# Performance work log

Measured on AMD Instinct MI355X. Metric: run time of the kernel, lower is better.

The kernel has to match this reference:

```python
import jax, jax.numpy as jnp
import numpy as np

H_DIM = 32
EPS = 1e-7


def setup_inputs() -> dict:
    key = jax.random.key(0)
    ks = jax.random.split(key, 9)
    B, L, I = 2048, 256, 8
    return {
        "X": jax.random.normal(ks[0], (B, L, I), dtype=jnp.float32),
        "y": jax.random.randint(ks[1], (B,), 0, 2, dtype=jnp.int64),
        "W1": jax.random.normal(ks[2], (I, H_DIM), dtype=jnp.float32),
        "cls_tok": jax.random.normal(ks[3], (H_DIM,), dtype=jnp.float32),
        "W_q": jax.random.normal(ks[4], (H_DIM, H_DIM), dtype=jnp.float32),
        "W_k": jax.random.normal(ks[5], (H_DIM, H_DIM), dtype=jnp.float32),
        "W_v": jax.random.normal(ks[6], (H_DIM, H_DIM), dtype=jnp.float32),
        "W_t": jax.random.normal(ks[7], (H_DIM, H_DIM), dtype=jnp.float32),
        "W2": jax.random.normal(ks[8], (H_DIM, 2), dtype=jnp.float32),
    }


def reference(X, y, W1, cls_tok, W_q, W_k, W_v, W_t, W2):
    B = X.shape[0]
    # global mean/std normalization (torch.std is unbiased, ddof=1)
    h_pre1 = (X - X.mean()) / (X.std(ddof=1) + EPS)
    h_1 = h_pre1 @ W1                                   # [B, L, H]
    cls = jnp.broadcast_to(cls_tok[None, None, :], (B, 1, H_DIM))
    h_pre2 = jnp.concatenate([h_1, cls], axis=1)        # [B, L+1, H]
    Q = h_pre2 @ W_q
    K = h_pre2 @ W_k
    V = h_pre2 @ W_v
    S = jax.nn.softmax(jnp.einsum('bqh,bkh->bqk', Q, K) / jnp.sqrt(jnp.float32(H_DIM)), axis=-1)
    h_2 = jnp.einsum('bqk,bkh->bqh', S, V) + h_pre2 @ W_t
    z = h_2[:, -1] @ W2                                 # [B, o_dim]
    log_s = jax.nn.log_softmax(z, axis=-1)
    loss = -jnp.take_along_axis(log_s, y[:, None], axis=1)[:, 0].mean()
    return loss
```

## Files before the change

### kernel.cpp

```cpp
#include <hip/hip_runtime.h>

#define N_TOTAL 4194304
#define B_SIZE  2048
#define L_SIZE  256
#define I_DIM   8
#define H       32
#define K1_BLK  256
#define K2_BLK  256

#define CRAW_OFF 1024
#define ACC_OFF  1040
#define FIXSCALE 4294967296.0
#define MASK56   0x00FFFFFFFFFFFFFFull

__global__ __launch_bounds__(1024) void k1_stats(
    const float4* __restrict__ X4,
    const float* __restrict__ W1, const float* __restrict__ cls,
    const float* __restrict__ Wq, const float* __restrict__ Wk,
    const float* __restrict__ Wv, const float* __restrict__ Wt,
    const float* __restrict__ W2, double* __restrict__ dws)
{
    const int t = threadIdx.x, b = blockIdx.x;
    const int lane = t & 63, wid = t >> 6;
    const int g = b * 1024 + t;

    float s1 = 0.f, s2 = 0.f;
    #pragma unroll
    for (int i = 0; i < 4; i++) {
        float4 v = X4[g + i * 262144];
        s1 += v.x + v.y + v.z + v.w;
        s2 += v.x * v.x + v.y * v.y + v.z * v.z + v.w * v.w;
    }
    for (int off = 32; off; off >>= 1) {
        s1 += __shfl_down(s1, off);
        s2 += __shfl_down(s2, off);
    }
    __shared__ float a1[16], a2[16];
    if (lane == 0) { a1[wid] = s1; a2[wid] = s2; }
    __syncthreads();
    if (t == 0) {
        float r1 = 0.f, r2 = 0.f;
        #pragma unroll
        for (int i = 0; i < 16; i++) { r1 += a1[i]; r2 += a2[i]; }
        dws[2 * b]     = (double)r1;
        dws[2 * b + 1] = (double)r2;
    }

    if (b == 0) {
        __shared__ float qv[H], kcls[H], vcls[H], tv[H], gg[H], WV[I_DIM][H];
        const float rs32 = 0.17677669529663687f;
        float* craw = (float*)(dws + CRAW_OFF);
        if (t < H) {
            const int h = t;
            float q_ = 0.f, k_ = 0.f, v_ = 0.f, t_ = 0.f;
            for (int j = 0; j < H; j++) {
                float cj = cls[j];
                q_ += cj * Wq[j * H + h];
                k_ += cj * Wk[j * H + h];
                v_ += cj * Wv[j * H + h];
                t_ += cj * Wt[j * H + h];
            }
            qv[h] = q_; kcls[h] = k_; vcls[h] = v_; tv[h] = t_;
        }
        __syncthreads();
        if (t < H) {
            const int h = t;
            float g_ = 0.f;
            for (int j = 0; j < H; j++) g_ += Wk[h * H + j] * qv[j];
            gg[h] = g_;
            for (int i = 0; i < I_DIM; i++) {
                float a = 0.f;
                for (int j = 0; j < H; j++) a += W1[i * H + j] * Wv[j * H + h];
                WV[i][h] = a;
            }
        }
        __syncthreads();
        if (t < I_DIM) {
            float a = 0.f;
            for (int j = 0; j < H; j++) a += W1[t * H + j] * gg[j];
            craw[t] = a;
        }
        if (t < I_DIM * 2) {
            const int i = t >> 1, o = t & 1;
            float a = 0.f;
            for (int j = 0; j < H; j++) a += WV[i][j] * W2[j * 2 + o];
            craw[10 + i * 2 + o] = a;
        }
        if (t == 0) {
            float c2 = 0.f;
            for (int j = 0; j < H; j++) c2 += qv[j] * kcls[j];
            craw[9] = c2 * rs32;
            float vw0 = 0.f, vw1 = 0.f, tw0 = 0.f, tw1 = 0.f;
            for (int j = 0; j < H; j++) {
                vw0 += vcls[j] * W2[j * 2];     vw1 += vcls[j] * W2[j * 2 + 1];
                tw0 += tv[j]   * W2[j * 2];     tw1 += tv[j]   * W2[j * 2 + 1];
            }
            craw[28] = vw0; craw[29] = vw1; craw[30] = tw0; craw[31] = tw1;
            *(unsigned long long*)(dws + ACC_OFF) = 0ull;
        }
    }
}

__global__ __launch_bounds__(1024) void k2_attn(
    const float* __restrict__ X, const int* __restrict__ y,
    double* __restrict__ dws, float* __restrict__ out)
{
    const int t = threadIdx.x, b = blockIdx.x;
    const int lane = t & 63, w = t >> 6;
    const int lr = w >> 1, half = w & 1;
    const int r = b * 8 + lr;

    const float4* Xb = (const float4*)X + (size_t)r * 512;
    const int p0 = half * 128 + lane;
    float4 A = Xb[2 * p0],        Bv = Xb[2 * p0 + 1];
    float4 C = Xb[2 * (p0 + 64)], D  = Xb[2 * (p0 + 64) + 1];

    __shared__ double da[4], db[4];
    if (t < 256) {
        double d1 = dws[2 * t], d2 = dws[2 * t + 1];
        for (int off = 32; off; off >>= 1) {
            d1 += __shfl_down(d1, off);
            d2 += __shfl_down(d2, off);
        }
        if (lane == 0) { da[w] = d1; db[w] = d2; }
    }
    __syncthreads();

    __shared__ float sNegMu, sSdev;
    if (t == 0) {
        double S1 = da[0] + da[1] + da[2] + da[3];
        double S2 = db[0] + db[1] + db[2] + db[3];
        double mu = S1 / (double)N_TOTAL;
        double var = (S2 - S1 * S1 / (double)N_TOTAL) / (double)(N_TOTAL - 1);
        sSdev = (float)(sqrt(var) + 1e-7);
        sNegMu = (float)(-mu);
    }
    __syncthreads();

    __shared__ float cst[32];
    const float* craw = (const float*)(dws + CRAW_OFF);
    const float rs32 = 0.17677669529663687f;
    if (t < 32) {
        const float sdev = sSdev, negmu = sNegMu;
        if (t < 8) {
            cst[t] = craw[t] / sdev * rs32;
        } else if (t == 8) {
            float cs = 0.f;
            for (int i = 0; i < 8; i++) cs += craw[i] / sdev * rs32;
            cst[8] = negmu * cs;
        } else if (t == 9) {
            cst[9] = craw[9];
        } else if (t < 26) {
            cst[t] = craw[t] / sdev;
        } else if (t == 26) {
            float m0 = 0.f;
            for (int i = 0; i < 8; i++) m0 += craw[10 + 2 * i] / sdev;
            cst[26] = negmu * m0;
        } else if (t == 27) {
            float m1 = 0.f;
            for (int i = 0; i < 8; i++) m1 += craw[11 + 2 * i] / sdev;
            cst[27] = negmu * m1;
        } else {
            cst[t] = craw[t];
        }
    }
    __syncthreads();

    float x0[8] = {A.x, A.y, A.z, A.w, Bv.x, Bv.y, Bv.z, Bv.w};
    float x1[8] = {C.x, C.y, C.z, C.w, D.x,  D.y,  D.z,  D.w};
    const float c8 = cst[8];
    float sc0 = c8, sc1 = c8;
    #pragma unroll
    for (int i = 0; i < 8; i++) {
        sc0 += x0[i] * cst[i];
        sc1 += x1[i] * cst[i];
    }

    __shared__ float rmax[8][2];
    __shared__ float rsum[8][2][9];
    __shared__ double wloss[8];
    float mw = fmaxf(sc0, sc1);
    for (int off = 32; off; off >>= 1) mw = fmaxf(mw, __shfl_xor(mw, off));
    if (lane == 0) rmax[lr][half] = mw;
    __syncthreads();
    const float m = fmaxf(fmaxf(rmax[lr][0], rmax[lr][1]), cst[9]);

    float e0 = expf(sc0 - m), e1 = expf(sc1 - m);
    float v[9];
    v[0] = e0 + e1;
    #pragma unroll
    for (int i = 0; i < 8; i++) v[i + 1] = e0 * x0[i] + e1 * x1[i];
    for (int off = 32; off; off >>= 1) {
        #pragma unroll
        for (int j = 0; j < 9; j++) v[j] += __shfl_down(v[j], off);
    }
    if (lane == 0) {
        #pragma unroll
        for (int j = 0; j < 9; j++) rsum[lr][half][j] = v[j];
    }
    __syncthreads();

    if (t < 8) {
        float vv[9];
        #pragma unroll
        for (int j = 0; j < 9; j++) vv[j] = rsum[t][0][j] + rsum[t][1][j];
        float mrow = fmaxf(fmaxf(rmax[t][0], rmax[t][1]), cst[9]);
        float ecls = expf(cst[9] - mrow);
        float inv = 1.f / (vv[0] + ecls);
        float S256 = ecls * inv;
        float z[2];
        #pragma unroll
        for (int o = 0; o < 2; o++) {
            float a = 0.f;
            #pragma unroll
            for (int i = 0; i < 8; i++)
                a += (vv[i + 1] * inv) * cst[10 + i * 2 + o];
            z[o] = a + (1.f - S256) * cst[26 + o] + S256 * cst[28 + o] + cst[30 + o];
        }
        float zm = fmaxf(z[0], z[1]);
        float lse = zm + logf(expf(z[0] - zm) + expf(z[1] - zm));
        int yb = y[b * 8 + t];
        wloss[t] = (double)(lse - z[yb]);
    }
    __syncthreads();

    if (t == 0) {
        double blockloss = 0.0;
        #pragma unroll
        for (int i = 0; i < 8; i++) blockloss += wloss[i];
        unsigned long long fixed =
            (unsigned long long)(blockloss * FIXSCALE + 0.5);
        unsigned long long* acc = (unsigned long long*)(dws + ACC_OFF);
        unsigned long long old = __hip_atomic_fetch_add(
            acc, fixed + (1ull << 56), __ATOMIC_RELAXED, __HIP_MEMORY_SCOPE_AGENT);
        if ((old >> 56) == (unsigned long long)(K2_BLK - 1)) {
            unsigned long long total = ((old & MASK56) + fixed) & MASK56;
            out[0] = (float)((double)total / FIXSCALE / (double)B_SIZE);
        }
    }
}

extern "C" void kernel_launch(void* const* d_in, const int* in_sizes, int n_in,
                              void* d_out, int out_size, void* d_ws, size_t ws_size,
                              hipStream_t stream) {
    const float* X   = (const float*)d_in[0];
    const int*   y   = (const int*)d_in[1];
    const float* W1  = (const float*)d_in[2];
    const float* cls = (const float*)d_in[3];
    const float* Wq  = (const float*)d_in[4];
    const float* Wk  = (const float*)d_in[5];
    const float* Wv  = (const float*)d_in[6];
    const float* Wt  = (const float*)d_in[7];
    const float* W2  = (const float*)d_in[8];
    float* out = (float*)d_out;
    double* dws = (double*)d_ws;

    hipLaunchKernelGGL(k1_stats, dim3(K1_BLK), dim3(1024), 0, stream,
                       (const float4*)X, W1, cls, Wq, Wk, Wv, Wt, W2, dws);
    hipLaunchKernelGGL(k2_attn, dim3(K2_BLK), dim3(1024), 0, stream,
                       X, y, dws, out);
}
```

Measured before the change: 23.02 us.

## Fuse stats and attention into one cooperative kernel with grid barrier

Merges the statistics pass and the attention/loss pass into a single cooperatively launched kernel. Each block loads its X rows into registers once, uses them for the global sum/sumsq, then waits on an atomic arrival counter before reusing the same registers for attention. This removes the second kernel launch and the second read of X. Every block now also recomputes the weight folding redundantly, and a memset is added to clear the counter. A two-kernel fallback with a 512-thread attention kernel is kept in case the cooperative launch fails.

```diff
diff --git a/kernel.cpp b/kernel.cpp
--- a/kernel.cpp
+++ b/kernel.cpp
@@ -5,143 +5,79 @@
 #define L_SIZE  256
 #define I_DIM   8
 #define H       32
-#define K1_BLK  256
-#define K2_BLK  256
-
-#define CRAW_OFF 1024
-#define ACC_OFF  1040
-#define FIXSCALE 4294967296.0
-#define MASK56   0x00FFFFFFFFFFFFFFull
-
-__global__ __launch_bounds__(1024) void k1_stats(
-    const float4* __restrict__ X4,
+#define NBLK    256
+
+#define ARR_BYTE  4160
+#define ACC_BYTE  4168
+#define CRAW_OFF  524
+#define FIXSCALE  4294967296.0
+#define MASK56    0x00FFFFFFFFFFFFFFull
+
+__device__ __forceinline__ void fold_raw(
+    int t,
     const float* __restrict__ W1, const float* __restrict__ cls,
     const float* __restrict__ Wq, const float* __restrict__ Wk,
     const float* __restrict__ Wv, const float* __restrict__ Wt,
-    const float* __restrict__ W2, double* __restrict__ dws)
+    const float* __restrict__ W2,
+    float* qv, float* kcls, float* vcls, float* tv, float* gg,
+    float (*WV)[H], float* craw)
 {
-    const int t = threadIdx.x, b = blockIdx.x;
-    const int lane = t & 63, wid = t >> 6;
-    const int g = b * 1024 + t;
-
-    float s1 = 0.f, s2 = 0.f;
-    #pragma unroll
-    for (int i = 0; i < 4; i++) {
-        float4 v = X4[g + i * 262144];
-        s1 += v.x + v.y + v.z + v.w;
-        s2 += v.x * v.x + v.y * v.y + v.z * v.z + v.w * v.w;
-    }
-    for (int off = 32; off; off >>= 1) {
-        s1 += __shfl_down(s1, off);
-        s2 += __shfl_down(s2, off);
-    }
-    __shared__ float a1[16], a2[16];
-    if (lane == 0) { a1[wid] = s1; a2[wid] = s2; }
-    __syncthreads();
-    if (t == 0) {
-        float r1 = 0.f, r2 = 0.f;
-        #pragma unroll
-        for (int i = 0; i < 16; i++) { r1 += a1[i]; r2 += a2[i]; }
-        dws[2 * b]     = (double)r1;
-        dws[2 * b + 1] = (double)r2;
-    }
-
-    if (b == 0) {
-        __shared__ float qv[H], kcls[H], vcls[H], tv[H], gg[H], WV[I_DIM][H];
-        const float rs32 = 0.17677669529663687f;
-        float* craw = (float*)(dws + CRAW_OFF);
-        if (t < H) {
-            const int h = t;
-            float q_ = 0.f, k_ = 0.f, v_ = 0.f, t_ = 0.f;
-            for (int j = 0; j < H; j++) {
-                float cj = cls[j];
-                q_ += cj * Wq[j * H + h];
-                k_ += cj * Wk[j * H + h];
-                v_ += cj * Wv[j * H + h];
-                t_ += cj * Wt[j * H + h];
-            }
-            qv[h] = q_; kcls[h] = k_; vcls[h] = v_; tv[h] = t_;
-        }
-        __syncthreads();
-        if (t < H) {
-            const int h = t;
-            float g_ = 0.f;
-            for (int j = 0; j < H; j++) g_ += Wk[h * H + j] * qv[j];
-            gg[h] = g_;
-            for (int i = 0; i < I_DIM; i++) {
-                float a = 0.f;
-                for (int j = 0; j < H; j++) a += W1[i * H + j] * Wv[j * H + h];
-                WV[i][h] = a;
-            }
-        }
-        __syncthreads();
-        if (t < I_DIM) {
+    const float rs32 = 0.17677669529663687f;
+    if (t < H) {
+        const int h = t;
+        float q_ = 0.f, k_ = 0.f, v_ = 0.f, t_ = 0.f;
+        for (int j = 0; j < H; j++) {
+            float cj = cls[j];
+            q_ += cj * Wq[j * H + h];
+            k_ += cj * Wk[j * H + h];
+            v_ += cj * Wv[j * H + h];
+            t_ += cj * Wt[j * H + h];
+        }
+        qv[h] = q_; kcls[h] = k_; vcls[h] = v_; tv[h] = t_;
+    }
+    __syncthreads();
+    if (t < H) {
+        const int h = t;
+        float g_ = 0.f;
+        for (int j = 0; j < H; j++) g_ += Wk[h * H + j] * qv[j];
+        gg[h] = g_;
+        for (int i = 0; i < I_DIM; i++) {
             float a = 0.f;
-            for (int j = 0; j < H; j++) a += W1[t * H + j] * gg[j];
-            craw[t] = a;
-        }
-        if (t < I_DIM * 2) {
-            const int i = t >> 1, o = t & 1;
-            float a = 0.f;
-            for (int j = 0; j < H; j++) a += WV[i][j] * W2[j * 2 + o];
-            craw[10 + i * 2 + o] = a;
-        }
-        if (t == 0) {
-            float c2 = 0.f;
-            for (int j = 0; j < H; j++) c2 += qv[j] * kcls[j];
-            craw[9] = c2 * rs32;
-            float vw0 = 0.f, vw1 = 0.f, tw0 = 0.f, tw1 = 0.f;
-            for (int j = 0; j < H; j++) {
-                vw0 += vcls[j] * W2[j * 2];     vw1 += vcls[j] * W2[j * 2 + 1];
-                tw0 += tv[j]   * W2[j * 2];     tw1 += tv[j]   * W2[j * 2 + 1];
-            }
-            craw[28] = vw0; craw[29] = vw1; craw[30] = tw0; craw[31] = tw1;
-            *(unsigned long long*)(dws + ACC_OFF) = 0ull;
-        }
-    }
-}
-
-__global__ __launch_bounds__(1024) void k2_attn(
-    const float* __restrict__ X, const int* __restrict__ y,
-    double* __restrict__ dws, float* __restrict__ out)
+            for (int j = 0; j < H; j++) a += W1[i * H + j] * Wv[j * H + h];
+            WV[i][h] = a;
+        }
+    }
+    __syncthreads();
+    if (t < I_DIM) {
+        float a = 0.f;
+        for (int j = 0; j < H; j++) a += W1[t * H + j] * gg[j];
+        craw[t] = a;
+    }
+    if (t < I_DIM * 2) {
+        const int i = t >> 1, o = t & 1;
+        float a = 0.f;
+        for (int j = 0; j < H; j++) a += WV[i][j] * W2[j * 2 + o];
+        craw[10 + i * 2 + o] = a;
+    }
+    if (t == 0) {
+        float c2 = 0.f;
+        for (int j = 0; j < H; j++) c2 += qv[j] * kcls[j];
+        craw[9] = c2 * rs32;
+        float vw0 = 0.f, vw1 = 0.f, tw0 = 0.f, tw1 = 0.f;
+        for (int j = 0; j < H; j++) {
+            vw0 += vcls[j] * W2[j * 2];     vw1 += vcls[j] * W2[j * 2 + 1];
+            tw0 += tv[j]   * W2[j * 2];     tw1 += tv[j]   * W2[j * 2 + 1];
+        }
+        craw[28] = vw0; craw[29] = vw1; craw[30] = tw0; craw[31] = tw1;
+    }
+    __syncthreads();
+}
+
+__device__ __forceinline__ void scale_cst(
+    int t, float negmu, float sdev, const float* craw, float* cst)
 {
-    const int t = threadIdx.x, b = blockIdx.x;
-    const int lane = t & 63, w = t >> 6;
-    const int lr = w >> 1, half = w & 1;
-    const int r = b * 8 + lr;
-
-    const float4* Xb = (const float4*)X + (size_t)r * 512;
-    const int p0 = half * 128 + lane;
-    float4 A = Xb[2 * p0],        Bv = Xb[2 * p0 + 1];
-    float4 C = Xb[2 * (p0 + 64)], D  = Xb[2 * (p0 + 64) + 1];
-
-    __shared__ double da[4], db[4];
-    if (t < 256) {
-        double d1 = dws[2 * t], d2 = dws[2 * t + 1];
-        for (int off = 32; off; off >>= 1) {
-            d1 += __shfl_down(d1, off);
-            d2 += __shfl_down(d2, off);
-        }
-        if (lane == 0) { da[w] = d1; db[w] = d2; }
-    }
-    __syncthreads();
-
-    __shared__ float sNegMu, sSdev;
-    if (t == 0) {
-        double S1 = da[0] + da[1] + da[2] + da[3];
-        double S2 = db[0] + db[1] + db[2] + db[3];
-        double mu = S1 / (double)N_TOTAL;
-        double var = (S2 - S1 * S1 / (double)N_TOTAL) / (double)(N_TOTAL - 1);
-        sSdev = (float)(sqrt(var) + 1e-7);
-        sNegMu = (float)(-mu);
-    }
-    __syncthreads();
-
-    __shared__ float cst[32];
-    const float* craw = (const float*)(dws + CRAW_OFF);
     const float rs32 = 0.17677669529663687f;
     if (t < 32) {
-        const float sdev = sSdev, negmu = sNegMu;
         if (t < 8) {
             cst[t] = craw[t] / sdev * rs32;
         } else if (t == 8) {
@@ -164,10 +100,95 @@
             cst[t] = craw[t];
         }
     }
-    __syncthreads();
-
+}
+
+__global__ __launch_bounds__(1024) void fused_coop(
+    const float* __restrict__ X, const int* __restrict__ y,
+    const float* __restrict__ W1, const float* __restrict__ cls,
+    const float* __restrict__ Wq, const float* __restrict__ Wk,
+    const float* __restrict__ Wv, const float* __restrict__ Wt,
+    const float* __restrict__ W2, float* __restrict__ out,
+    double* __restrict__ dws)
+{
+    const int t = threadIdx.x, b = blockIdx.x;
+    const int lane = t & 63, w = t >> 6;
+    const int lr = w >> 1, half = w & 1;
+    const int r = b * 8 + lr;
+
+    const float4* Xb = (const float4*)X + (size_t)r * 512;
+    const int p0 = half * 128 + lane;
+    float4 A = Xb[2 * p0],        Bv = Xb[2 * p0 + 1];
+    float4 C = Xb[2 * (p0 + 64)], D  = Xb[2 * (p0 + 64) + 1];
     float x0[8] = {A.x, A.y, A.z, A.w, Bv.x, Bv.y, Bv.z, Bv.w};
     float x1[8] = {C.x, C.y, C.z, C.w, D.x,  D.y,  D.z,  D.w};
+
+    float s1 = 0.f, s2 = 0.f;
+    #pragma unroll
+    for (int i = 0; i < 8; i++) {
+        s1 += x0[i] + x1[i];
+        s2 += x0[i] * x0[i] + x1[i] * x1[i];
+    }
+    for (int off = 32; off; off >>= 1) {
+        s1 += __shfl_down(s1, off);
+        s2 += __shfl_down(s2, off);
+    }
+    __shared__ float a1[16], a2[16];
+    if (lane == 0) { a1[w] = s1; a2[w] = s2; }
+    __syncthreads();
+
+    unsigned* arrive = (unsigned*)((char*)dws + ARR_BYTE);
+    if (t == 0) {
+        float r1 = 0.f, r2 = 0.f;
+        #pragma unroll
+        for (int i = 0; i < 16; i++) { r1 += a1[i]; r2 += a2[i]; }
+        __hip_atomic_store(&dws[2 * b], (double)r1,
+                           __ATOMIC_RELEASE, __HIP_MEMORY_SCOPE_AGENT);
+        __hip_atomic_store(&dws[2 * b + 1], (double)r2,
+                           __ATOMIC_RELEASE, __HIP_MEMORY_SCOPE_AGENT);
+        __hip_atomic_fetch_add(arrive, 1u, __ATOMIC_RELEASE,
+                               __HIP_MEMORY_SCOPE_AGENT);
+    }
+
+    __shared__ float qv[H], kcls[H], vcls[H], tv[H], gg[H], WV[I_DIM][H];
+    __shared__ float craw[32];
+    fold_raw(t, W1, cls, Wq, Wk, Wv, Wt, W2, qv, kcls, vcls, tv, gg, WV, craw);
+
+    if (t == 0) {
+        while (__hip_atomic_load(arrive, __ATOMIC_ACQUIRE,
+                                 __HIP_MEMORY_SCOPE_AGENT) < (unsigned)NBLK)
+            __builtin_amdgcn_s_sleep(2);
+    }
+    __syncthreads();
+
+    __shared__ double da[4], db[4];
+    if (t < 256) {
+        double d1 = __hip_atomic_load(&dws[2 * t], __ATOMIC_RELAXED,
+                                      __HIP_MEMORY_SCOPE_AGENT);
+        double d2 = __hip_atomic_load(&dws[2 * t + 1], __ATOMIC_RELAXED,
+                                      __HIP_MEMORY_SCOPE_AGENT);
+        for (int off = 32; off; off >>= 1) {
+            d1 += __shfl_down(d1, off);
+            d2 += __shfl_down(d2, off);
+        }
+        if (lane == 0) { da[w] = d1; db[w] = d2; }
+    }
+    __syncthreads();
+
+    __shared__ float sNegMu, sSdev;
+    if (t == 0) {
+        double S1 = da[0] + da[1] + da[2] + da[3];
+        double S2 = db[0] + db[1] + db[2] + db[3];
+        double mu = S1 / (double)N_TOTAL;
+        double var = (S2 - S1 * S1 / (double)N_TOTAL) / (double)(N_TOTAL - 1);
+        sSdev = (float)(sqrt(var) + 1e-7);
+        sNegMu = (float)(-mu);
+    }
+    __syncthreads();
+
+    __shared__ float cst[32];
+    scale_cst(t, sNegMu, sSdev, craw, cst);
+    __syncthreads();
+
     const float c8 = cst[8];
     float sc0 = c8, sc1 = c8;
     #pragma unroll
@@ -230,10 +251,153 @@
         for (int i = 0; i < 8; i++) blockloss += wloss[i];
         unsigned long long fixed =
             (unsigned long long)(blockloss * FIXSCALE + 0.5);
-        unsigned long long* acc = (unsigned long long*)(dws + ACC_OFF);
+        unsigned long long* acc = (unsigned long long*)((char*)dws + ACC_BYTE);
         unsigned long long old = __hip_atomic_fetch_add(
             acc, fixed + (1ull << 56), __ATOMIC_RELAXED, __HIP_MEMORY_SCOPE_AGENT);
-        if ((old >> 56) == (unsigned long long)(K2_BLK - 1)) {
+        if ((old >> 56) == (unsigned long long)(NBLK - 1)) {
+            unsigned long long total = ((old & MASK56) + fixed) & MASK56;
+            out[0] = (float)((double)total / FIXSCALE / (double)B_SIZE);
+        }
+    }
+}
+
+__global__ __launch_bounds__(1024) void k1_stats(
+    const float4* __restrict__ X4,
+    const float* __restrict__ W1, const float* __restrict__ cls,
+    const float* __restrict__ Wq, const float* __restrict__ Wk,
+    const float* __restrict__ Wv, const float* __restrict__ Wt,
+    const float* __restrict__ W2, double* __restrict__ dws)
+{
+    const int t = threadIdx.x, b = blockIdx.x;
+    const int lane = t & 63, wid = t >> 6;
+    const int g = b * 1024 + t;
+
+    float s1 = 0.f, s2 = 0.f;
+    #pragma unroll
+    for (int i = 0; i < 4; i++) {
+        float4 v = X4[g + i * 262144];
+        s1 += v.x + v.y + v.z + v.w;
+        s2 += v.x * v.x + v.y * v.y + v.z * v.z + v.w * v.w;
+    }
+    for (int off = 32; off; off >>= 1) {
+        s1 += __shfl_down(s1, off);
+        s2 += __shfl_down(s2, off);
+    }
+    __shared__ float a1[16], a2[16];
+    if (lane == 0) { a1[wid] = s1; a2[wid] = s2; }
+    __syncthreads();
+    if (t == 0) {
+        float r1 = 0.f, r2 = 0.f;
+        #pragma unroll
+        for (int i = 0; i < 16; i++) { r1 += a1[i]; r2 += a2[i]; }
+        dws[2 * b]     = (double)r1;
+        dws[2 * b + 1] = (double)r2;
+    }
+    if (b == 0) {
+        __shared__ float qv[H], kcls[H], vcls[H], tv[H], gg[H], WV[I_DIM][H];
+        float* craw = (float*)(dws + CRAW_OFF);
+        fold_raw(t, W1, cls, Wq, Wk, Wv, Wt, W2, qv, kcls, vcls, tv, gg, WV, craw);
+    }
+}
+
+__global__ __launch_bounds__(512) void k2_attn(
+    const float* __restrict__ X, const int* __restrict__ y,
+    double* __restrict__ dws, float* __restrict__ out)
+{
+    const int t = threadIdx.x, b = blockIdx.x;
+    const int lane = t & 63, w = t >> 6;
+
+    __shared__ double da[4], db[4];
+    __shared__ float cst[32];
+    __shared__ double wloss[8];
+
+    if (t < 256) {
+        double d1 = dws[2 * t], d2 = dws[2 * t + 1];
+        for (int off = 32; off; off >>= 1) {
+            d1 += __shfl_down(d1, off);
+            d2 += __shfl_down(d2, off);
+        }
+        if (lane == 0) { da[w] = d1; db[w] = d2; }
+    }
+    __syncthreads();
+    __shared__ float sNegMu, sSdev;
+    if (t == 0) {
+        double S1 = da[0] + da[1] + da[2] + da[3];
+        double S2 = db[0] + db[1] + db[2] + db[3];
+        double mu = S1 / (double)N_TOTAL;
+        double var = (S2 - S1 * S1 / (double)N_TOTAL) / (double)(N_TOTAL - 1);
+        sSdev = (float)(sqrt(var) + 1e-7);
+        sNegMu = (float)(-mu);
+    }
+    __syncthreads();
+    scale_cst(t, sNegMu, sSdev, (const float*)(dws + CRAW_OFF), cst);
+    __syncthreads();
+
+    const int r = b * 8 + w;
+    const float4* Xb = (const float4*)X + (size_t)r * 512;
+    float x[4][8];
+    float sc[4];
+    const float c8 = cst[8];
+    #pragma unroll
+    for (int j = 0; j < 4; j++) {
+        const int p = 64 * j + lane;
+        float4 p0 = Xb[2 * p], p1 = Xb[2 * p + 1];
+        x[j][0] = p0.x; x[j][1] = p0.y; x[j][2] = p0.z; x[j][3] = p0.w;
+        x[j][4] = p1.x; x[j][5] = p1.y; x[j][6] = p1.z; x[j][7] = p1.w;
+        float s = c8;
+        #pragma unroll
+        for (int i = 0; i < 8; i++) s += x[j][i] * cst[i];
+        sc[j] = s;
+    }
+    float m = fmaxf(fmaxf(sc[0], sc[1]), fmaxf(sc[2], sc[3]));
+    for (int off = 32; off; off >>= 1) m = fmaxf(m, __shfl_xor(m, off));
+    m = fmaxf(m, cst[9]);
+
+    float v[9];
+    #pragma unroll
+    for (int j2 = 0; j2 < 9; j2++) v[j2] = 0.f;
+    #pragma unroll
+    for (int j = 0; j < 4; j++) {
+        float e = expf(sc[j] - m);
+        v[0] += e;
+        #pragma unroll
+        for (int i = 0; i < 8; i++) v[i + 1] += e * x[j][i];
+    }
+    for (int off = 32; off; off >>= 1) {
+        #pragma unroll
+        for (int j2 = 0; j2 < 9; j2++) v[j2] += __shfl_down(v[j2], off);
+    }
+    if (lane == 0) {
+        float se = v[0];
+        float ecls = expf(cst[9] - m);
+        float inv = 1.f / (se + ecls);
+        float S256 = ecls * inv;
+        float z[2];
+        #pragma unroll
+        for (int o = 0; o < 2; o++) {
+            float a = 0.f;
+            #pragma unroll
+            for (int i = 0; i < 8; i++)
+                a += (v[i + 1] * inv) * cst[10 + i * 2 + o];
+            z[o] = a + (1.f - S256) * cst[26 + o] + S256 * cst[28 + o] + cst[30 + o];
+        }
+        float zm = fmaxf(z[0], z[1]);
+        float lse = zm + logf(expf(z[0] - zm) + expf(z[1] - zm));
+        int yb = y[r];
+        wloss[w] = (double)(lse - z[yb]);
+    }
+    __syncthreads();
+
+    if (t == 0) {
+        double blockloss = 0.0;
+        #pragma unroll
+        for (int i = 0; i < 8; i++) blockloss += wloss[i];
+        unsigned long long fixed =
+            (unsigned long long)(blockloss * FIXSCALE + 0.5);
+        unsigned long long* acc = (unsigned long long*)((char*)dws + ACC_BYTE);
+        unsigned long long old = __hip_atomic_fetch_add(
+            acc, fixed + (1ull << 56), __ATOMIC_RELAXED, __HIP_MEMORY_SCOPE_AGENT);
+        if ((old >> 56) == 255ull) {
             unsigned long long total = ((old & MASK56) + fixed) & MASK56;
             out[0] = (float)((double)total / FIXSCALE / (double)B_SIZE);
         }
@@ -255,8 +419,18 @@
     float* out = (float*)d_out;
     double* dws = (double*)d_ws;
 
-    hipLaunchKernelGGL(k1_stats, dim3(K1_BLK), dim3(1024), 0, stream,
-                       (const float4*)X, W1, cls, Wq, Wk, Wv, Wt, W2, dws);
-    hipLaunchKernelGGL(k2_attn, dim3(K2_BLK), dim3(1024), 0, stream,
-                       X, y, dws, out);
-}
+    hipMemsetAsync((char*)d_ws + ARR_BYTE, 0, 16, stream);
+
+    void* args[] = {(void*)&X, (void*)&y, (void*)&W1, (void*)&cls,
+                    (void*)&Wq, (void*)&Wk, (void*)&Wv, (void*)&Wt,
+                    (void*)&W2, (void*)&out, (void*)&dws};
+    hipError_t err = hipLaunchCooperativeKernel(
+        reinterpret_cast<void*>(fused_coop), dim3(NBLK), dim3(1024), args, 0, stream);
+
+    if (err != hipSuccess) {
+        hipLaunchKernelGGL(k1_stats, dim3(256), dim3(1024), 0, stream,
+                           (const float4*)X, W1, cls, Wq, Wk, Wv, Wt, W2, dws);
+        hipLaunchKernelGGL(k2_attn, dim3(256), dim3(512), 0, stream,
+                           X, y, dws, out);
+    }
+}
```

New measurement: 50.33 us. 2.19x slower.
